# Kernel optimization log

Hardware: AMD Instinct MI355X
Metric: run time of the kernel (lower is better)

The kernel has to match this reference:

```python
import jax, jax.numpy as jnp
import numpy as np

B = 2048          # batch_size from init
D = 512           # embedding dim
TAU = 0.5         # temperature
EPS = 1e-12       # torch F.normalize eps


def _l2_normalize(x):
    n = jnp.linalg.norm(x, axis=1, keepdims=True)
    return x / jnp.maximum(n, EPS)


def setup_inputs() -> dict:
    key = jax.random.key(0)
    k1, k2 = jax.random.split(key)
    emb_i = jax.random.normal(k1, (2 * B, D), dtype=jnp.float32)
    emb_j = jax.random.normal(k2, (2 * B, D), dtype=jnp.float32)
    return {"emb_i": emb_i, "emb_j": emb_j}


def reference(emb_i, emb_j):
    z_i = _l2_normalize(emb_i)
    z_j = _l2_normalize(emb_j)
    rep = jnp.concatenate([z_i, z_j], axis=0)        # [4B, D], unit rows
    # cosine similarity of unit vectors == plain GEMM
    sim = rep @ rep.T                                # [4B, 4B]
    n = 4 * B
    pos1 = jnp.concatenate([jnp.diagonal(sim, B), jnp.diagonal(sim, -B)])        # [6B]
    pos2 = jnp.concatenate([jnp.diagonal(sim, 2 * B), jnp.diagonal(sim, -2 * B)])  # [4B]
    pos3 = jnp.concatenate([jnp.diagonal(sim, 3 * B), jnp.diagonal(sim, -3 * B)])  # [2B]
    nominator = (jnp.sum(jnp.exp(pos1 / TAU))
                 + jnp.sum(jnp.exp(pos2 / TAU))
                 + jnp.sum(jnp.exp(pos3 / TAU)))
    off_diag = 1.0 - jnp.eye(n, dtype=sim.dtype)
    denominator = jnp.sum(off_diag * jnp.exp(sim / TAU)) - nominator
    loss = -jnp.log(nominator / denominator) / (4 * B)
    return loss
```

## Files before the change

### kernel.cpp

```cpp
#include <hip/hip_runtime.h>
#include <stdint.h>
#include <math.h>

#define DIM       512
#define NROWS     8192
#define HALF_ROWS 4096
#define NT        32
#define NTRI      528
#define NXCD      8
#define TPX       66
#define GRID_G    512

typedef float  floatx16 __attribute__((ext_vector_type(16)));
typedef __bf16 bf16x8   __attribute__((ext_vector_type(8)));

__device__ __forceinline__ void async_copy16(const unsigned short* g, unsigned short* l) {
    __builtin_amdgcn_global_load_lds(
        (const __attribute__((address_space(1))) uint32_t*)(g),
        (__attribute__((address_space(3))) uint32_t*)(l),
        16, 0, 0);
}

__global__ __launch_bounds__(256) void normalize_kernel(
    const float* __restrict__ emb_i, const float* __restrict__ emb_j,
    unsigned short* __restrict__ rep, double* __restrict__ ws)
{
    if (blockIdx.x == 0 && threadIdx.x == 0) {
        ws[0] = 0.0; ws[1] = 0.0;
        ((unsigned long long*)ws)[2] = 0ull;
    }
    const int wave = threadIdx.x >> 6;
    const int lane = threadIdx.x & 63;
    const int row  = blockIdx.x * 4 + wave;
    const float* src = (row < HALF_ROWS) ? (emb_i + (size_t)row * DIM)
                                         : (emb_j + (size_t)(row - HALF_ROWS) * DIM);
    const int c = lane * 8;
    float4 v0 = *(const float4*)(src + c);
    float4 v1 = *(const float4*)(src + c + 4);
    float s = v0.x*v0.x + v0.y*v0.y + v0.z*v0.z + v0.w*v0.w
            + v1.x*v1.x + v1.y*v1.y + v1.z*v1.z + v1.w*v1.w;
    #pragma unroll
    for (int off = 32; off; off >>= 1) s += __shfl_xor(s, off, 64);
    const float inv = 1.0f / fmaxf(sqrtf(s), 1e-12f);
    float f[8] = {v0.x*inv, v0.y*inv, v0.z*inv, v0.w*inv,
                  v1.x*inv, v1.y*inv, v1.z*inv, v1.w*inv};
    union { unsigned short h[8]; uint4 u; } pk;
    #pragma unroll
    for (int t = 0; t < 8; ++t) {
        uint32_t b = __float_as_uint(f[t]);
        b += 0x7FFFu + ((b >> 16) & 1u);
        pk.h[t] = (unsigned short)(b >> 16);
    }
    *(uint4*)(rep + (size_t)row * DIM + c) = pk.u;
}

__device__ __forceinline__ void stage_half(const unsigned short* __restrict__ rep,
    int rowbase, int k0, unsigned short* lds, int tid)
{
    #pragma unroll
    for (int l = 0; l < 2; ++l) {
        const int ch  = l * 512 + tid;
        const int row = ch >> 3;
        const int s   = ch & 7;
        const int col = (s ^ (row & 7)) << 3;
        async_copy16(rep + (size_t)(rowbase + row) * DIM + (k0 + col), lds + ch * 8);
    }
}

#define PH_BAR1() do { __builtin_amdgcn_s_barrier(); \
    asm volatile("s_waitcnt lgkmcnt(0)" ::: "memory"); \
    __builtin_amdgcn_sched_barrier(0); } while (0)

#define PH_BAR2() do { __builtin_amdgcn_s_barrier(); \
    __builtin_amdgcn_sched_barrier(0); } while (0)

#define WAIT_VM(N) asm volatile("s_waitcnt vmcnt(" #N ")" ::: "memory")

#define LOAD_A(BUF, MH) do { const unsigned short* Ah_ = sA[BUF][wm]; \
    _Pragma("unroll") for (int mt = 0; mt < 2; ++mt) { \
        const char* rp_ = (const char*)Ah_ + ((MH)*64 + mt*32 + r32) * 128; \
        _Pragma("unroll") for (int kf = 0; kf < 4; ++kf) \
            a[mt][kf] = *(const bf16x8*)(rp_ + ((kf*32 + half16) ^ swz)); } } while (0)

#define LOAD_B(BUF, NJ, DST) do { const unsigned short* Bh_ = sB[BUF][wn >> 1]; \
    const char* rp_ = (const char*)Bh_ + (((wn & 1)*64 + (NJ)*32 + r32) * 128); \
    _Pragma("unroll") for (int kf = 0; kf < 4; ++kf) \
        DST[kf] = *(const bf16x8*)(rp_ + ((kf*32 + half16) ^ swz)); } while (0)

#define MFMA_Q(MH, NJ, BB) do { \
    __builtin_amdgcn_s_setprio(1); \
    _Pragma("unroll") for (int mt = 0; mt < 2; ++mt) \
      _Pragma("unroll") for (int kf = 0; kf < 4; ++kf) \
        acc[(MH)*2 + mt][NJ] = __builtin_amdgcn_mfma_f32_32x32x16_bf16( \
            a[mt][kf], BB[kf], acc[(MH)*2 + mt][NJ], 0, 0, 0); \
    __builtin_amdgcn_s_setprio(0); } while (0)

__global__ __launch_bounds__(512, 2) void gram_kernel(
    const unsigned short* __restrict__ rep, double* __restrict__ ws,
    float* __restrict__ out)
{
    __shared__ unsigned short sA[2][2][128 * 64];
    __shared__ unsigned short sB[2][2][128 * 64];
    __shared__ float red[16];

    const int tid  = threadIdx.x;
    const int wave = tid >> 6, lane = tid & 63;
    const int wm = wave >> 2, wn = wave & 3;
    const int r32 = lane & 31, half16 = (lane >> 5) * 16;
    const int swz = (r32 & 7) << 4;

    const int x = blockIdx.x & 7, slot = blockIdx.x >> 3;
    int u_first, ntile;
    if (slot < 2) { u_first = x * TPX + slot * 2; ntile = 2; }
    else          { u_first = x * TPX + slot + 2; ntile = 1; }

    for (int t = 0; t < ntile; ++t) {
        const int u = u_first + t;
        int bi = (int)((2.0f * NT + 1.0f
                 - sqrtf((2.0f * NT + 1.0f) * (2.0f * NT + 1.0f) - 8.0f * (float)u)) * 0.5f);
        while ((bi + 1) * NT - ((bi + 1) * bi) / 2 <= u) ++bi;
        while (bi * NT - (bi * (bi - 1)) / 2 > u) --bi;
        const int bj = bi + (u - (bi * NT - (bi * (bi - 1)) / 2));
        const int i0 = bi * 256, j0 = bj * 256;

        floatx16 acc[4][2];
        #pragma unroll
        for (int p = 0; p < 4; ++p)
            #pragma unroll
            for (int q = 0; q < 2; ++q)
                #pragma unroll
                for (int e = 0; e < 16; ++e) acc[p][q][e] = 0.0f;

        bf16x8 a[2][4], bL[4], bR[4];

        stage_half(rep, i0,       0,  sA[0][0], tid);
        stage_half(rep, i0 + 128, 0,  sA[0][1], tid);
        stage_half(rep, j0,       0,  sB[0][0], tid);
        stage_half(rep, j0 + 128, 0,  sB[0][1], tid);
        stage_half(rep, j0,       64, sB[1][0], tid);
        stage_half(rep, j0 + 128, 64, sB[1][1], tid);
        WAIT_VM(4);
        __builtin_amdgcn_s_barrier();
        __builtin_amdgcn_sched_barrier(0);

        int kA1 = 64, kT2 = 128, kT3 = 192;
        for (int it = 0; it < 3; ++it) {
            LOAD_A(0, 0); LOAD_B(0, 0, bL);
            stage_half(rep, i0, kA1, sA[1][0], tid);
            PH_BAR1(); MFMA_Q(0, 0, bL); PH_BAR2();
            LOAD_B(0, 1, bR);
            stage_half(rep, i0 + 128, kA1, sA[1][1], tid);
            PH_BAR1(); MFMA_Q(0, 1, bR); PH_BAR2();
            LOAD_A(0, 1);
            stage_half(rep, j0, kT2, sB[0][0], tid);
            PH_BAR1(); MFMA_Q(1, 1, bR); PH_BAR2();
            stage_half(rep, j0 + 128, kT2, sB[0][1], tid);
            WAIT_VM(4);
            PH_BAR1(); MFMA_Q(1, 0, bL); PH_BAR2();
            LOAD_A(1, 0); LOAD_B(1, 0, bL);
            stage_half(rep, i0, kT2, sA[0][0], tid);
            PH_BAR1(); MFMA_Q(0, 0, bL); PH_BAR2();
            LOAD_B(1, 1, bR);
            stage_half(rep, i0 + 128, kT2, sA[0][1], tid);
            PH_BAR1(); MFMA_Q(0, 1, bR); PH_BAR2();
            LOAD_A(1, 1);
            stage_half(rep, j0, kT3, sB[1][0], tid);
            PH_BAR1(); MFMA_Q(1, 1, bR); PH_BAR2();
            stage_half(rep, j0 + 128, kT3, sB[1][1], tid);
            WAIT_VM(4);
            PH_BAR1(); MFMA_Q(1, 0, bL); PH_BAR2();
            kA1 += 128; kT2 += 128; kT3 += 128;
        }

        LOAD_A(0, 0); LOAD_B(0, 0, bL);
        stage_half(rep, i0, 448, sA[1][0], tid);
        PH_BAR1(); MFMA_Q(0, 0, bL); PH_BAR2();
        LOAD_B(0, 1, bR);
        stage_half(rep, i0 + 128, 448, sA[1][1], tid);
        PH_BAR1(); MFMA_Q(0, 1, bR); PH_BAR2();
        LOAD_A(0, 1);
        PH_BAR1(); MFMA_Q(1, 1, bR); PH_BAR2();
        WAIT_VM(0);
        PH_BAR1(); MFMA_Q(1, 0, bL); PH_BAR2();
        LOAD_A(1, 0); LOAD_B(1, 0, bL);
        PH_BAR1(); MFMA_Q(0, 0, bL); PH_BAR2();
        LOAD_B(1, 1, bR);
        PH_BAR1(); MFMA_Q(0, 1, bR); PH_BAR2();
        LOAD_A(1, 1);
        PH_BAR1(); MFMA_Q(1, 1, bR); PH_BAR2();
        MFMA_Q(1, 0, bL);

        float s_all = 0.0f, s_pos = 0.0f;
        const float LOG2E2 = 2.885390081777927f;
        const int rbase = (half16 >> 2);
        #pragma unroll
        for (int mi = 0; mi < 4; ++mi) {
            const int ib = i0 + wm * 128 + mi * 32 + rbase;
            #pragma unroll
            for (int nj = 0; nj < 2; ++nj) {
                const int j = j0 + wn * 64 + nj * 32 + r32;
                const floatx16 v = acc[mi][nj];
                #pragma unroll
                for (int reg = 0; reg < 16; ++reg) {
                    const int i = ib + (reg & 3) + 8 * (reg >> 2);
                    const float ex = exp2f(v[reg] * LOG2E2);
                    if (i != j) s_all += ex;
                    const int d = j - i;
                    if (d == 2048 || d == 4096 || d == 6144) s_pos += ex;
                }
            }
        }
        #pragma unroll
        for (int off = 32; off; off >>= 1) {
            s_all += __shfl_xor(s_all, off, 64);
            s_pos += __shfl_xor(s_pos, off, 64);
        }
        if (lane == 0) { red[wave] = s_all; red[8 + wave] = s_pos; }
        __syncthreads();
        if (tid == 0) {
            float ta = 0.0f, tp = 0.0f;
            #pragma unroll
            for (int w2 = 0; w2 < 8; ++w2) { ta += red[w2]; tp += red[8 + w2]; }
            const float wgt = (bi == bj) ? 1.0f : 2.0f;
            atomicAdd(&ws[0], (double)(ta * wgt));
            atomicAdd(&ws[1], (double)(tp * wgt));
            __threadfence();
            unsigned* ctr = (unsigned*)(ws + 2);
            const unsigned done = atomicAdd(ctr, 1u);
            if (done == NTRI - 1) {
                __threadfence();
                const double nom = atomicAdd(&ws[1], 0.0);
                const double den = atomicAdd(&ws[0], 0.0) - nom;
                out[0] = (float)(-log(nom / den) / (double)NROWS);
            }
        }
        __syncthreads();
    }
}

extern "C" void kernel_launch(void* const* d_in, const int* in_sizes, int n_in,
                              void* d_out, int out_size, void* d_ws, size_t ws_size,
                              hipStream_t stream) {
    const float* emb_i = (const float*)d_in[0];
    const float* emb_j = (const float*)d_in[1];
    float* out = (float*)d_out;
    double* ws = (double*)d_ws;
    unsigned short* rep = (unsigned short*)((char*)d_ws + 256);

    hipLaunchKernelGGL(normalize_kernel, dim3(NROWS / 4), dim3(256), 0, stream,
                       emb_i, emb_j, rep, ws);
    hipLaunchKernelGGL(gram_kernel, dim3(GRID_G), dim3(512), 0, stream, rep, ws, out);
}
```

Measured before the change: 152.5 us.

## Launch one workgroup per triangle tile with XCD-aware block-to-tile mapping

Replaces the old persistent schedule, where 512 blocks handled one or two tiles each, with a 528-block grid that gives each block exactly one upper-triangular 256x256 tile. Tiles are assigned per XCD with a hand-built mapping: 10 tiles from the XCD's own 4x4 diagonal block group, plus off-diagonal tiles from a round-robin pairing of XCD groups, so rows stay resident in each XCD's L2. It also drops the min-2-blocks-per-CU launch bound. The single-tile-per-block layout removes the tile loop and the triangular index arithmetic, but it relies on blocks being dispatched round-robin across the 8 XCDs and makes the last wave of blocks uneven.

```diff
diff --git a/kernel.cpp b/kernel.cpp
--- a/kernel.cpp
+++ b/kernel.cpp
@@ -7,9 +7,7 @@
 #define HALF_ROWS 4096
 #define NT        32
 #define NTRI      528
-#define NXCD      8
-#define TPX       66
-#define GRID_G    512
+#define GRID_G    528
 
 typedef float  floatx16 __attribute__((ext_vector_type(16)));
 typedef __bf16 bf16x8   __attribute__((ext_vector_type(8)));
@@ -95,7 +93,7 @@
             a[mt][kf], BB[kf], acc[(MH)*2 + mt][NJ], 0, 0, 0); \
     __builtin_amdgcn_s_setprio(0); } while (0)
 
-__global__ __launch_bounds__(512, 2) void gram_kernel(
+__global__ __launch_bounds__(512) void gram_kernel(
     const unsigned short* __restrict__ rep, double* __restrict__ ws,
     float* __restrict__ out)
 {
@@ -109,132 +107,135 @@
     const int r32 = lane & 31, half16 = (lane >> 5) * 16;
     const int swz = (r32 & 7) << 4;
 
-    const int x = blockIdx.x & 7, slot = blockIdx.x >> 3;
-    int u_first, ntile;
-    if (slot < 2) { u_first = x * TPX + slot * 2; ntile = 2; }
-    else          { u_first = x * TPX + slot + 2; ntile = 1; }
-
-    for (int t = 0; t < ntile; ++t) {
-        const int u = u_first + t;
-        int bi = (int)((2.0f * NT + 1.0f
-                 - sqrtf((2.0f * NT + 1.0f) * (2.0f * NT + 1.0f) - 8.0f * (float)u)) * 0.5f);
-        while ((bi + 1) * NT - ((bi + 1) * bi) / 2 <= u) ++bi;
-        while (bi * NT - (bi * (bi - 1)) / 2 > u) --bi;
-        const int bj = bi + (u - (bi * NT - (bi * (bi - 1)) / 2));
-        const int i0 = bi * 256, j0 = bj * 256;
-
-        floatx16 acc[4][2];
+    const int x = blockIdx.x & 7;
+    const int t = blockIdx.x >> 3;
+    int bi, bj;
+    if (t < 10) {
+        const int a = (0xE9500 >> (2 * t)) & 3;
+        const int b = (0xFBEE4 >> (2 * t)) & 3;
+        bi = x * 4 + a;  bj = x * 4 + b;
+    } else {
+        const int r = (t - 10) >> 3, k = (t - 10) & 7;
+        int p;
+        if (x == 7) p = r;
+        else if (x == r) p = 7;
+        else { p = (2 * r - x + 7) % 7; }
+        const int g = (x < p) ? x : p, h = (x < p) ? p : x;
+        const int m16 = (x == g) ? k : 8 + k;
+        bi = g * 4 + (m16 >> 2);  bj = h * 4 + (m16 & 3);
+    }
+    const int i0 = bi * 256, j0 = bj * 256;
+
+    floatx16 acc[4][2];
+    #pragma unroll
+    for (int p2 = 0; p2 < 4; ++p2)
         #pragma unroll
-        for (int p = 0; p < 4; ++p)
+        for (int q = 0; q < 2; ++q)
             #pragma unroll
-            for (int q = 0; q < 2; ++q)
-                #pragma unroll
-                for (int e = 0; e < 16; ++e) acc[p][q][e] = 0.0f;
-
-        bf16x8 a[2][4], bL[4], bR[4];
-
-        stage_half(rep, i0,       0,  sA[0][0], tid);
-        stage_half(rep, i0 + 128, 0,  sA[0][1], tid);
-        stage_half(rep, j0,       0,  sB[0][0], tid);
-        stage_half(rep, j0 + 128, 0,  sB[0][1], tid);
-        stage_half(rep, j0,       64, sB[1][0], tid);
-        stage_half(rep, j0 + 128, 64, sB[1][1], tid);
-        WAIT_VM(4);
-        __builtin_amdgcn_s_barrier();
-        __builtin_amdgcn_sched_barrier(0);
-
-        int kA1 = 64, kT2 = 128, kT3 = 192;
-        for (int it = 0; it < 3; ++it) {
-            LOAD_A(0, 0); LOAD_B(0, 0, bL);
-            stage_half(rep, i0, kA1, sA[1][0], tid);
-            PH_BAR1(); MFMA_Q(0, 0, bL); PH_BAR2();
-            LOAD_B(0, 1, bR);
-            stage_half(rep, i0 + 128, kA1, sA[1][1], tid);
-            PH_BAR1(); MFMA_Q(0, 1, bR); PH_BAR2();
-            LOAD_A(0, 1);
-            stage_half(rep, j0, kT2, sB[0][0], tid);
-            PH_BAR1(); MFMA_Q(1, 1, bR); PH_BAR2();
-            stage_half(rep, j0 + 128, kT2, sB[0][1], tid);
-            WAIT_VM(4);
-            PH_BAR1(); MFMA_Q(1, 0, bL); PH_BAR2();
-            LOAD_A(1, 0); LOAD_B(1, 0, bL);
-            stage_half(rep, i0, kT2, sA[0][0], tid);
-            PH_BAR1(); MFMA_Q(0, 0, bL); PH_BAR2();
-            LOAD_B(1, 1, bR);
-            stage_half(rep, i0 + 128, kT2, sA[0][1], tid);
-            PH_BAR1(); MFMA_Q(0, 1, bR); PH_BAR2();
-            LOAD_A(1, 1);
-            stage_half(rep, j0, kT3, sB[1][0], tid);
-            PH_BAR1(); MFMA_Q(1, 1, bR); PH_BAR2();
-            stage_half(rep, j0 + 128, kT3, sB[1][1], tid);
-            WAIT_VM(4);
-            PH_BAR1(); MFMA_Q(1, 0, bL); PH_BAR2();
-            kA1 += 128; kT2 += 128; kT3 += 128;
-        }
-
+            for (int e = 0; e < 16; ++e) acc[p2][q][e] = 0.0f;
+
+    bf16x8 a[2][4], bL[4], bR[4];
+
+    stage_half(rep, i0,       0,  sA[0][0], tid);
+    stage_half(rep, i0 + 128, 0,  sA[0][1], tid);
+    stage_half(rep, j0,       0,  sB[0][0], tid);
+    stage_half(rep, j0 + 128, 0,  sB[0][1], tid);
+    stage_half(rep, j0,       64, sB[1][0], tid);
+    stage_half(rep, j0 + 128, 64, sB[1][1], tid);
+    WAIT_VM(4);
+    __builtin_amdgcn_s_barrier();
+    __builtin_amdgcn_sched_barrier(0);
+
+    int kA1 = 64, kT2 = 128, kT3 = 192;
+    for (int it = 0; it < 3; ++it) {
         LOAD_A(0, 0); LOAD_B(0, 0, bL);
-        stage_half(rep, i0, 448, sA[1][0], tid);
+        stage_half(rep, i0, kA1, sA[1][0], tid);
         PH_BAR1(); MFMA_Q(0, 0, bL); PH_BAR2();
         LOAD_B(0, 1, bR);
-        stage_half(rep, i0 + 128, 448, sA[1][1], tid);
+        stage_half(rep, i0 + 128, kA1, sA[1][1], tid);
         PH_BAR1(); MFMA_Q(0, 1, bR); PH_BAR2();
         LOAD_A(0, 1);
+        stage_half(rep, j0, kT2, sB[0][0], tid);
         PH_BAR1(); MFMA_Q(1, 1, bR); PH_BAR2();
-        WAIT_VM(0);
+        stage_half(rep, j0 + 128, kT2, sB[0][1], tid);
+        WAIT_VM(4);
         PH_BAR1(); MFMA_Q(1, 0, bL); PH_BAR2();
         LOAD_A(1, 0); LOAD_B(1, 0, bL);
+        stage_half(rep, i0, kT2, sA[0][0], tid);
         PH_BAR1(); MFMA_Q(0, 0, bL); PH_BAR2();
         LOAD_B(1, 1, bR);
+        stage_half(rep, i0 + 128, kT2, sA[0][1], tid);
         PH_BAR1(); MFMA_Q(0, 1, bR); PH_BAR2();
         LOAD_A(1, 1);
+        stage_half(rep, j0, kT3, sB[1][0], tid);
         PH_BAR1(); MFMA_Q(1, 1, bR); PH_BAR2();
-        MFMA_Q(1, 0, bL);
-
-        float s_all = 0.0f, s_pos = 0.0f;
-        const float LOG2E2 = 2.885390081777927f;
-        const int rbase = (half16 >> 2);
+        stage_half(rep, j0 + 128, kT3, sB[1][1], tid);
+        WAIT_VM(4);
+        PH_BAR1(); MFMA_Q(1, 0, bL); PH_BAR2();
+        kA1 += 128; kT2 += 128; kT3 += 128;
+    }
+
+    LOAD_A(0, 0); LOAD_B(0, 0, bL);
+    stage_half(rep, i0, 448, sA[1][0], tid);
+    PH_BAR1(); MFMA_Q(0, 0, bL); PH_BAR2();
+    LOAD_B(0, 1, bR);
+    stage_half(rep, i0 + 128, 448, sA[1][1], tid);
+    PH_BAR1(); MFMA_Q(0, 1, bR); PH_BAR2();
+    LOAD_A(0, 1);
+    PH_BAR1(); MFMA_Q(1, 1, bR); PH_BAR2();
+    WAIT_VM(0);
+    PH_BAR1(); MFMA_Q(1, 0, bL); PH_BAR2();
+    LOAD_A(1, 0); LOAD_B(1, 0, bL);
+    PH_BAR1(); MFMA_Q(0, 0, bL); PH_BAR2();
+    LOAD_B(1, 1, bR);
+    PH_BAR1(); MFMA_Q(0, 1, bR); PH_BAR2();
+    LOAD_A(1, 1);
+    PH_BAR1(); MFMA_Q(1, 1, bR); PH_BAR2();
+    MFMA_Q(1, 0, bL);
+
+    float s_all = 0.0f, s_pos = 0.0f;
+    const float LOG2E2 = 2.885390081777927f;
+    const int rbase = (half16 >> 2);
+    #pragma unroll
+    for (int mi = 0; mi < 4; ++mi) {
+        const int ib = i0 + wm * 128 + mi * 32 + rbase;
         #pragma unroll
-        for (int mi = 0; mi < 4; ++mi) {
-            const int ib = i0 + wm * 128 + mi * 32 + rbase;
+        for (int nj = 0; nj < 2; ++nj) {
+            const int j = j0 + wn * 64 + nj * 32 + r32;
+            const floatx16 v = acc[mi][nj];
             #pragma unroll
-            for (int nj = 0; nj < 2; ++nj) {
-                const int j = j0 + wn * 64 + nj * 32 + r32;
-                const floatx16 v = acc[mi][nj];
-                #pragma unroll
-                for (int reg = 0; reg < 16; ++reg) {
-                    const int i = ib + (reg & 3) + 8 * (reg >> 2);
-                    const float ex = exp2f(v[reg] * LOG2E2);
-                    if (i != j) s_all += ex;
-                    const int d = j - i;
-                    if (d == 2048 || d == 4096 || d == 6144) s_pos += ex;
-                }
+            for (int reg = 0; reg < 16; ++reg) {
+                const int i = ib + (reg & 3) + 8 * (reg >> 2);
+                const float ex = exp2f(v[reg] * LOG2E2);
+                if (i != j) s_all += ex;
+                const int d = j - i;
+                if (d == 2048 || d == 4096 || d == 6144) s_pos += ex;
             }
         }
+    }
+    #pragma unroll
+    for (int off = 32; off; off >>= 1) {
+        s_all += __shfl_xor(s_all, off, 64);
+        s_pos += __shfl_xor(s_pos, off, 64);
+    }
+    if (lane == 0) { red[wave] = s_all; red[8 + wave] = s_pos; }
+    __syncthreads();
+    if (tid == 0) {
+        float ta = 0.0f, tp = 0.0f;
         #pragma unroll
-        for (int off = 32; off; off >>= 1) {
-            s_all += __shfl_xor(s_all, off, 64);
-            s_pos += __shfl_xor(s_pos, off, 64);
+        for (int w2 = 0; w2 < 8; ++w2) { ta += red[w2]; tp += red[8 + w2]; }
+        const float wgt = (bi == bj) ? 1.0f : 2.0f;
+        atomicAdd(&ws[0], (double)(ta * wgt));
+        atomicAdd(&ws[1], (double)(tp * wgt));
+        __threadfence();
+        unsigned* ctr = (unsigned*)(ws + 2);
+        const unsigned done = atomicAdd(ctr, 1u);
+        if (done == NTRI - 1) {
+            __threadfence();
+            const double nom = atomicAdd(&ws[1], 0.0);
+            const double den = atomicAdd(&ws[0], 0.0) - nom;
+            out[0] = (float)(-log(nom / den) / (double)NROWS);
         }
-        if (lane == 0) { red[wave] = s_all; red[8 + wave] = s_pos; }
-        __syncthreads();
-        if (tid == 0) {
-            float ta = 0.0f, tp = 0.0f;
-            #pragma unroll
-            for (int w2 = 0; w2 < 8; ++w2) { ta += red[w2]; tp += red[8 + w2]; }
-            const float wgt = (bi == bj) ? 1.0f : 2.0f;
-            atomicAdd(&ws[0], (double)(ta * wgt));
-            atomicAdd(&ws[1], (double)(tp * wgt));
-            __threadfence();
-            unsigned* ctr = (unsigned*)(ws + 2);
-            const unsigned done = atomicAdd(ctr, 1u);
-            if (done == NTRI - 1) {
-                __threadfence();
-                const double nom = atomicAdd(&ws[1], 0.0);
-                const double den = atomicAdd(&ws[0], 0.0) - nom;
-                out[0] = (float)(-log(nom / den) / (double)NROWS);
-            }
-        }
-        __syncthreads();
     }
 }
 
```

Result: no change. 150.3 us (-1.5%).
